# Kernel tuning notes

Measured on AMD Instinct MI355X. Metric: run time of the kernel, lower is better.

The kernel has to match this reference:

```python
import jax, jax.numpy as jnp
import numpy as np

NUM_BUYERS = 1024
BATCH = 16384
K, J = 2, 3


def setup_inputs() -> dict:
    key = jax.random.key(0)
    k1, k2, k3 = jax.random.split(key, 3)
    bids = jax.random.uniform(k1, (BATCH, NUM_BUYERS), dtype=jnp.float32)
    w_params = jax.random.normal(k2, (NUM_BUYERS, K, J), dtype=jnp.float32)
    beta_params = jax.random.normal(k3, (NUM_BUYERS, K, J), dtype=jnp.float32)
    return {"bids": bids, "w_params": w_params, "beta_params": beta_params}


def reference(bids, w_params, beta_params):
    # linear_funcs[b, i, k, j] = bids[b, i] * exp(w[i, k, j]) + beta[i, k, j]
    w = jnp.exp(w_params)                                   # [N, K, J]
    linear_funcs = bids[:, :, None, None] * w[None] + beta_params[None]  # [B, N, K, J]
    max_over_j = jnp.max(linear_funcs, axis=3)              # [B, N, K]
    virtual_values = jnp.min(max_over_j, axis=2)            # [B, N]
    return virtual_values
```

## Files before the change

kernel.cpp:

```cpp
#include <hip/hip_runtime.h>


#define NB    1024
#define BATCH 16384
#define KK    2
#define JJ    3
#define ROWS  8
#define COLS_PER_BLOCK 512

__global__ __launch_bounds__(256, 8) void vvn_kernel(
    const float* __restrict__ bids,
    const float* __restrict__ w,
    const float* __restrict__ beta,
    float* __restrict__ out)
{
    const int t       = threadIdx.x;
    const int colHalf = blockIdx.x & 1;
    const int stripe  = blockIdx.x >> 1;
    const int i0      = colHalf * COLS_PER_BLOCK + (t << 1);

    float ew[2][KK][JJ];
    float bt[2][KK][JJ];
#pragma unroll
    for (int u = 0; u < 2; ++u) {
        const int base = (i0 + u) * (KK * JJ);
#pragma unroll
        for (int k = 0; k < KK; ++k) {
#pragma unroll
            for (int j = 0; j < JJ; ++j) {
                ew[u][k][j] = __expf(w[base + k * JJ + j]);
                bt[u][k][j] = beta[base + k * JJ + j];
            }
        }
    }

    const size_t b0   = (size_t)stripe * ROWS;
    const size_t base = b0 * NB + i0;

    float2 bv[ROWS];
#pragma unroll
    for (int r = 0; r < ROWS; ++r) {
        bv[r] = *reinterpret_cast<const float2*>(&bids[base + (size_t)r * NB]);
    }

#pragma unroll
    for (int r = 0; r < ROWS; ++r) {
        const float a0 = bv[r].x;
        const float a1 = bv[r].y;

        float m00 = fmaf(a0, ew[0][0][0], bt[0][0][0]);
        m00 = fmaxf(m00, fmaf(a0, ew[0][0][1], bt[0][0][1]));
        m00 = fmaxf(m00, fmaf(a0, ew[0][0][2], bt[0][0][2]));
        float m01 = fmaf(a0, ew[0][1][0], bt[0][1][0]);
        m01 = fmaxf(m01, fmaf(a0, ew[0][1][1], bt[0][1][1]));
        m01 = fmaxf(m01, fmaf(a0, ew[0][1][2], bt[0][1][2]));

        float m10 = fmaf(a1, ew[1][0][0], bt[1][0][0]);
        m10 = fmaxf(m10, fmaf(a1, ew[1][0][1], bt[1][0][1]));
        m10 = fmaxf(m10, fmaf(a1, ew[1][0][2], bt[1][0][2]));
        float m11 = fmaf(a1, ew[1][1][0], bt[1][1][0]);
        m11 = fmaxf(m11, fmaf(a1, ew[1][1][1], bt[1][1][1]));
        m11 = fmaxf(m11, fmaf(a1, ew[1][1][2], bt[1][1][2]));

        *reinterpret_cast<float2*>(&out[base + (size_t)r * NB]) =
            make_float2(fminf(m00, m01), fminf(m10, m11));
    }
}

extern "C" void kernel_launch(void* const* d_in, const int* in_sizes, int n_in,
                              void* d_out, int out_size, void* d_ws, size_t ws_size,
                              hipStream_t stream) {
    const float* bids = (const float*)d_in[0];
    const float* w    = (const float*)d_in[1];
    const float* beta = (const float*)d_in[2];
    float* out = (float*)d_out;

    vvn_kernel<<<dim3((BATCH / ROWS) * 2), dim3(256), 0, stream>>>(bids, w, beta, out);
}
```

Measured before the change: 25.05 us.

## Use float4 per-thread columns, nontemporal bid loads/stores, and vectorized param loads

Each thread now handles four adjacent buyer columns with 16-byte vector loads and stores, and one block covers a full 1024-wide row group of 4 rows instead of half-row stripes of 8 rows. Bids are loaded before the parameters so the streaming traffic is issued early. Bid loads and output stores are marked nontemporal to avoid polluting cache with streaming data. The w/beta parameters are fetched as six float4 vectors per thread. This raises per-thread register use (24 exps, more parameter registers), which the launch bound is lowered to accommodate at the cost of occupancy.

```diff
diff --git a/kernel.cpp b/kernel.cpp
--- a/kernel.cpp
+++ b/kernel.cpp
@@ -1,69 +1,70 @@
 #include <hip/hip_runtime.h>
 
+
+typedef float f4 __attribute__((ext_vector_type(4)));
 
 #define NB    1024
 #define BATCH 16384
 #define KK    2
 #define JJ    3
-#define ROWS  8
-#define COLS_PER_BLOCK 512
+#define ROWS  4
 
-__global__ __launch_bounds__(256, 8) void vvn_kernel(
+__global__ __launch_bounds__(256, 5) void vvn_kernel(
     const float* __restrict__ bids,
     const float* __restrict__ w,
     const float* __restrict__ beta,
     float* __restrict__ out)
 {
-    const int t       = threadIdx.x;
-    const int colHalf = blockIdx.x & 1;
-    const int stripe  = blockIdx.x >> 1;
-    const int i0      = colHalf * COLS_PER_BLOCK + (t << 1);
+    const int t  = threadIdx.x;
+    const int i0 = t << 2;
+    const size_t base = (size_t)blockIdx.x * ROWS * NB + i0;
 
-    float ew[2][KK][JJ];
-    float bt[2][KK][JJ];
+    f4 bv[ROWS];
 #pragma unroll
-    for (int u = 0; u < 2; ++u) {
-        const int base = (i0 + u) * (KK * JJ);
+    for (int r = 0; r < ROWS; ++r) {
+        bv[r] = __builtin_nontemporal_load(
+            reinterpret_cast<const f4*>(&bids[base + (size_t)r * NB]));
+    }
+
+    f4 wv[6], bb[6];
+    {
+        const f4* wp = reinterpret_cast<const f4*>(w    + (size_t)i0 * (KK * JJ));
+        const f4* bp = reinterpret_cast<const f4*>(beta + (size_t)i0 * (KK * JJ));
+#pragma unroll
+        for (int q = 0; q < 6; ++q) { wv[q] = wp[q]; bb[q] = bp[q]; }
+    }
+
+    float ew[4][KK][JJ];
+    float bt[4][KK][JJ];
+#pragma unroll
+    for (int u = 0; u < 4; ++u) {
 #pragma unroll
         for (int k = 0; k < KK; ++k) {
 #pragma unroll
             for (int j = 0; j < JJ; ++j) {
-                ew[u][k][j] = __expf(w[base + k * JJ + j]);
-                bt[u][k][j] = beta[base + k * JJ + j];
+                const int idx = u * (KK * JJ) + k * JJ + j;
+                ew[u][k][j] = __expf(reinterpret_cast<const float*>(wv)[idx]);
+                bt[u][k][j] = reinterpret_cast<const float*>(bb)[idx];
             }
         }
     }
 
-    const size_t b0   = (size_t)stripe * ROWS;
-    const size_t base = b0 * NB + i0;
-
-    float2 bv[ROWS];
 #pragma unroll
     for (int r = 0; r < ROWS; ++r) {
-        bv[r] = *reinterpret_cast<const float2*>(&bids[base + (size_t)r * NB]);
-    }
-
+        f4 res;
 #pragma unroll
-    for (int r = 0; r < ROWS; ++r) {
-        const float a0 = bv[r].x;
-        const float a1 = bv[r].y;
-
-        float m00 = fmaf(a0, ew[0][0][0], bt[0][0][0]);
-        m00 = fmaxf(m00, fmaf(a0, ew[0][0][1], bt[0][0][1]));
-        m00 = fmaxf(m00, fmaf(a0, ew[0][0][2], bt[0][0][2]));
-        float m01 = fmaf(a0, ew[0][1][0], bt[0][1][0]);
-        m01 = fmaxf(m01, fmaf(a0, ew[0][1][1], bt[0][1][1]));
-        m01 = fmaxf(m01, fmaf(a0, ew[0][1][2], bt[0][1][2]));
-
-        float m10 = fmaf(a1, ew[1][0][0], bt[1][0][0]);
-        m10 = fmaxf(m10, fmaf(a1, ew[1][0][1], bt[1][0][1]));
-        m10 = fmaxf(m10, fmaf(a1, ew[1][0][2], bt[1][0][2]));
-        float m11 = fmaf(a1, ew[1][1][0], bt[1][1][0]);
-        m11 = fmaxf(m11, fmaf(a1, ew[1][1][1], bt[1][1][1]));
-        m11 = fmaxf(m11, fmaf(a1, ew[1][1][2], bt[1][1][2]));
-
-        *reinterpret_cast<float2*>(&out[base + (size_t)r * NB]) =
-            make_float2(fminf(m00, m01), fminf(m10, m11));
+        for (int u = 0; u < 4; ++u) {
+            const float a = bv[r][u];
+            float m0 = fmaf(a, ew[u][0][0], bt[u][0][0]);
+            m0 = fmaxf(m0, fmaf(a, ew[u][0][1], bt[u][0][1]));
+            m0 = fmaxf(m0, fmaf(a, ew[u][0][2], bt[u][0][2]));
+            float m1 = fmaf(a, ew[u][1][0], bt[u][1][0]);
+            m1 = fmaxf(m1, fmaf(a, ew[u][1][1], bt[u][1][1]));
+            m1 = fmaxf(m1, fmaf(a, ew[u][1][2], bt[u][1][2]));
+            res[u] = fminf(m0, m1);
+        }
+        __builtin_nontemporal_store(
+            res, reinterpret_cast<f4*>(&out[base + (size_t)r * NB]));
     }
 }
 
@@ -75,5 +76,5 @@
     const float* beta = (const float*)d_in[2];
     float* out = (float*)d_out;
 
-    vvn_kernel<<<dim3((BATCH / ROWS) * 2), dim3(256), 0, stream>>>(bids, w, beta, out);
+    vvn_kernel<<<dim3(BATCH / ROWS), dim3(256), 0, stream>>>(bids, w, beta, out);
 }
```

Result: slower. 37.89 us (+51.3%).

## Process two row stripes per block and vectorize parameter loads

Applied to the files above, without the earlier changes.

Halves the grid so each block handles two 8-row stripes, reusing the exp'd weights and beta across both stripes instead of recomputing them per block. Parameter loads become three 16-byte vector loads per array, and the first stripe's bids loads are issued before the parameter loads to overlap latency. This trades fewer blocks, and so less parallelism to hide memory latency, for less redundant exp and parameter traffic.

```diff
diff --git a/kernel.cpp b/kernel.cpp
--- a/kernel.cpp
+++ b/kernel.cpp
@@ -1,12 +1,14 @@
 #include <hip/hip_runtime.h>
 
 
+typedef float f2 __attribute__((ext_vector_type(2)));
+typedef float f4 __attribute__((ext_vector_type(4)));
+
 #define NB    1024
 #define BATCH 16384
-#define KK    2
-#define JJ    3
 #define ROWS  8
-#define COLS_PER_BLOCK 512
+#define HALF  512
+#define NSTRIPE 1024
 
 __global__ __launch_bounds__(256, 8) void vvn_kernel(
     const float* __restrict__ bids,
@@ -14,56 +16,64 @@
     const float* __restrict__ beta,
     float* __restrict__ out)
 {
-    const int t       = threadIdx.x;
-    const int colHalf = blockIdx.x & 1;
-    const int stripe  = blockIdx.x >> 1;
-    const int i0      = colHalf * COLS_PER_BLOCK + (t << 1);
+    const int t  = threadIdx.x;
+    const int h  = blockIdx.x & 1;
+    const int s0 = blockIdx.x >> 1;
+    const int i0 = h * HALF + (t << 1);
 
-    float ew[2][KK][JJ];
-    float bt[2][KK][JJ];
+    const size_t baseA = (size_t)s0 * (ROWS * NB) + i0;
+
+    f2 bv[ROWS];
 #pragma unroll
-    for (int u = 0; u < 2; ++u) {
-        const int base = (i0 + u) * (KK * JJ);
+    for (int r = 0; r < ROWS; ++r)
+        bv[r] = *reinterpret_cast<const f2*>(&bids[baseA + (size_t)r * NB]);
+
+    float ew[2][2][3], bt[2][2][3];
+    {
+        const f4* wp = reinterpret_cast<const f4*>(w    + (size_t)i0 * 6);
+        const f4* bp = reinterpret_cast<const f4*>(beta + (size_t)i0 * 6);
+        f4 wv[3], bb[3];
 #pragma unroll
-        for (int k = 0; k < KK; ++k) {
+        for (int q = 0; q < 3; ++q) { wv[q] = wp[q]; bb[q] = bp[q]; }
 #pragma unroll
-            for (int j = 0; j < JJ; ++j) {
-                ew[u][k][j] = __expf(w[base + k * JJ + j]);
-                bt[u][k][j] = beta[base + k * JJ + j];
-            }
-        }
-    }
-
-    const size_t b0   = (size_t)stripe * ROWS;
-    const size_t base = b0 * NB + i0;
-
-    float2 bv[ROWS];
+        for (int u = 0; u < 2; ++u)
 #pragma unroll
-    for (int r = 0; r < ROWS; ++r) {
-        bv[r] = *reinterpret_cast<const float2*>(&bids[base + (size_t)r * NB]);
+            for (int k = 0; k < 2; ++k)
+#pragma unroll
+                for (int j = 0; j < 3; ++j) {
+                    const int idx = u * 6 + k * 3 + j;
+                    ew[u][k][j] = __expf(wv[idx >> 2][idx & 3]);
+                    bt[u][k][j] = bb[idx >> 2][idx & 3];
+                }
     }
 
 #pragma unroll
-    for (int r = 0; r < ROWS; ++r) {
-        const float a0 = bv[r].x;
-        const float a1 = bv[r].y;
-
-        float m00 = fmaf(a0, ew[0][0][0], bt[0][0][0]);
-        m00 = fmaxf(m00, fmaf(a0, ew[0][0][1], bt[0][0][1]));
-        m00 = fmaxf(m00, fmaf(a0, ew[0][0][2], bt[0][0][2]));
-        float m01 = fmaf(a0, ew[0][1][0], bt[0][1][0]);
-        m01 = fmaxf(m01, fmaf(a0, ew[0][1][1], bt[0][1][1]));
-        m01 = fmaxf(m01, fmaf(a0, ew[0][1][2], bt[0][1][2]));
-
-        float m10 = fmaf(a1, ew[1][0][0], bt[1][0][0]);
-        m10 = fmaxf(m10, fmaf(a1, ew[1][0][1], bt[1][0][1]));
-        m10 = fmaxf(m10, fmaf(a1, ew[1][0][2], bt[1][0][2]));
-        float m11 = fmaf(a1, ew[1][1][0], bt[1][1][0]);
-        m11 = fmaxf(m11, fmaf(a1, ew[1][1][1], bt[1][1][1]));
-        m11 = fmaxf(m11, fmaf(a1, ew[1][1][2], bt[1][1][2]));
-
-        *reinterpret_cast<float2*>(&out[base + (size_t)r * NB]) =
-            make_float2(fminf(m00, m01), fminf(m10, m11));
+    for (int it = 0; it < 2; ++it) {
+        const size_t base = baseA + (size_t)it * ((size_t)NSTRIPE * ROWS * NB);
+        if (it == 1) {
+#pragma unroll
+            for (int r = 0; r < ROWS; ++r)
+                bv[r] = *reinterpret_cast<const f2*>(&bids[base + (size_t)r * NB]);
+        }
+#pragma unroll
+        for (int r = 0; r < ROWS; ++r) {
+            const float a0 = bv[r][0];
+            const float a1 = bv[r][1];
+            float m00 = fmaf(a0, ew[0][0][0], bt[0][0][0]);
+            m00 = fmaxf(m00, fmaf(a0, ew[0][0][1], bt[0][0][1]));
+            m00 = fmaxf(m00, fmaf(a0, ew[0][0][2], bt[0][0][2]));
+            float m01 = fmaf(a0, ew[0][1][0], bt[0][1][0]);
+            m01 = fmaxf(m01, fmaf(a0, ew[0][1][1], bt[0][1][1]));
+            m01 = fmaxf(m01, fmaf(a0, ew[0][1][2], bt[0][1][2]));
+            float m10 = fmaf(a1, ew[1][0][0], bt[1][0][0]);
+            m10 = fmaxf(m10, fmaf(a1, ew[1][0][1], bt[1][0][1]));
+            m10 = fmaxf(m10, fmaf(a1, ew[1][0][2], bt[1][0][2]));
+            float m11 = fmaf(a1, ew[1][1][0], bt[1][1][0]);
+            m11 = fmaxf(m11, fmaf(a1, ew[1][1][1], bt[1][1][1]));
+            m11 = fmaxf(m11, fmaf(a1, ew[1][1][2], bt[1][1][2]));
+            f2 res; res[0] = fminf(m00, m01); res[1] = fminf(m10, m11);
+            *reinterpret_cast<f2*>(&out[base + (size_t)r * NB]) = res;
+        }
     }
 }
 
@@ -75,5 +85,5 @@
     const float* beta = (const float*)d_in[2];
     float* out = (float*)d_out;
 
-    vvn_kernel<<<dim3((BATCH / ROWS) * 2), dim3(256), 0, stream>>>(bids, w, beta, out);
+    vvn_kernel<<<dim3(2 * NSTRIPE), dim3(256), 0, stream>>>(bids, w, beta, out);
 }
```

Measured after the change: 25.47 us. About the same (+1.7%).
